# Kernel tuning notes

Measured on AMD Instinct MI355X. Metric: run time of the kernel, lower is better.

The kernel has to match this reference:

```python
import jax, jax.numpy as jnp
import numpy as np

Q = 12
DEGREE = 3
N_CONTROL = 25
N_POINTS = 500000
INPUT_DIM = 256


def make_open_uniform_knots(n_control, degree):
    n_knots = n_control + degree + 1
    n_internal = n_knots - 2 * (degree + 1)
    internal = np.linspace(0.0, 1.0, n_internal + 2)[1:-1]
    knots = np.concatenate([np.zeros(degree + 1), internal, np.ones(degree + 1)])
    return jnp.asarray(knots, dtype=jnp.float32)


def bspline_basis(x, knots, degree, n_basis):
    # x: [M] in [0,1]; returns [M, n_basis] via vectorized Cox-de Boor recursion
    x = jnp.clip(x, knots[0], knots[-1])
    xe = x[:, None]                      # [M,1]
    left = knots[:n_basis]
    right = knots[1:n_basis + 1]
    is_last = jnp.arange(n_basis) == (n_basis - 1)
    # degree-0 indicator; last interval is closed on the right
    N = jnp.where(is_last,
                  (xe >= left) & (xe <= right),
                  (xe >= left) & (xe < right)).astype(x.dtype)
    for p in range(1, degree + 1):
        d1 = knots[p:p + n_basis] - knots[:n_basis]
        d2 = knots[p + 1:p + 1 + n_basis] - knots[1:1 + n_basis]
        safe1 = jnp.where(d1 != 0, d1, 1.0)
        safe2 = jnp.where(d2 != 0, d2, 1.0)
        c1 = jnp.where(d1 != 0, (xe - knots[:n_basis]) / safe1, 0.0)
        c2 = jnp.where(d2 != 0, (knots[p + 1:p + 1 + n_basis] - xe) / safe2, 0.0)
        N_shift = jnp.concatenate([N[:, 1:], jnp.zeros_like(N[:, :1])], axis=1)
        N = c1 * N + c2 * N_shift
    return N


def setup_inputs() -> dict:
    key = jax.random.key(0)
    k0, k1, k2, k3 = jax.random.split(key, 4)
    emb = jax.random.normal(k0, (N_POINTS, INPUT_DIM), jnp.float32)
    W = jax.random.normal(k1, (Q, INPUT_DIM), jnp.float32) * 0.05
    b_inner = jnp.zeros((Q,), jnp.float32)
    inner_scale = jnp.full((1,), 0.5, jnp.float32)
    coeffs = jax.random.normal(k2, (Q, N_CONTROL), jnp.float32) * 0.05
    a = jax.random.normal(k3, (Q, 1), jnp.float32) * 0.05
    b_out = jnp.zeros((1,), jnp.float32)
    return {"emb": emb, "W": W, "b_inner": b_inner, "inner_scale": inner_scale,
            "coeffs": coeffs, "a": a, "b_out": b_out}


def reference(emb, W, b_inner, inner_scale, coeffs, a, b_out):
    knots = make_open_uniform_knots(N_CONTROL, DEGREE)  # constant buffer
    u_inner = emb @ W.T + b_inner                       # [N,Q]
    s = 0.5 * (jnp.tanh(inner_scale * u_inner) + 1.0)   # [N,Q] in (0,1)
    B_flat = bspline_basis(s.reshape(-1), knots, DEGREE, N_CONTROL)  # [N*Q, C]
    B = B_flat.reshape(emb.shape[0], Q, N_CONTROL)
    phi = jnp.einsum('nqc,qc->nq', B, coeffs)           # [N,Q]
    u_out = phi @ a + b_out                             # [N,1]
    return u_out
```

## Files before the change

kernel.cpp:

```cpp
#include <hip/hip_runtime.h>
#include <hip/hip_bf16.h>
#include <math.h>

#define NQ 12
#define DIMK 256
#define NCTRL 25
#define TPB 256
#define PTS_PER_BLK 256

__global__ __launch_bounds__(TPB, 4) void kan_bspline_kernel(
    const float* __restrict__ emb,
    const float* __restrict__ W,
    const float* __restrict__ b_inner,
    const float* __restrict__ inner_scale,
    const float* __restrict__ coeffs,
    const float* __restrict__ a_out,
    const float* __restrict__ b_out,
    float* __restrict__ out,
    int n)
{
    __shared__ __align__(16) float sW[NQ * DIMK];
    __shared__ float sC[NQ * NCTRL];

    for (int i = threadIdx.x; i < NQ * DIMK / 4; i += TPB)
        ((float4*)sW)[i] = ((const float4*)W)[i];
    for (int i = threadIdx.x; i < NQ * NCTRL; i += TPB)
        sC[i] = coeffs[i];
    __syncthreads();

    const int lane_r = threadIdx.x & 3;
    const int grp    = threadIdx.x >> 2;
    const int p0     = blockIdx.x * PTS_PER_BLK + grp * 4;
    const int nm1    = n - 1;

    float acc[NQ][4];
    #pragma unroll
    for (int q = 0; q < NQ; ++q)
        #pragma unroll
        for (int p = 0; p < 4; ++p)
            acc[q][p] = 0.0f;

    #pragma unroll 4
    for (int i = 0; i < 16; ++i) {
        const int k = lane_r * 4 + i * 16;
        float4 e[4];
        #pragma unroll
        for (int p = 0; p < 4; ++p) {
            int pi = p0 + p;
            pi = pi > nm1 ? nm1 : pi;
            e[p] = *(const float4*)(emb + (size_t)pi * DIMK + k);
        }
        #pragma unroll
        for (int q = 0; q < NQ; ++q) {
            float4 w = *(const float4*)(sW + q * DIMK + k);
            #pragma unroll
            for (int p = 0; p < 4; ++p) {
                acc[q][p] += e[p].x * w.x;
                acc[q][p] += e[p].y * w.y;
                acc[q][p] += e[p].z * w.z;
                acc[q][p] += e[p].w * w.w;
            }
        }
    }

    float u[NQ];
    #pragma unroll
    for (int q = 0; q < NQ; ++q) {
        float s0 = acc[q][0] + __shfl_xor(acc[q][0], 1);
        float s1 = acc[q][1] + __shfl_xor(acc[q][1], 1);
        float s2 = acc[q][2] + __shfl_xor(acc[q][2], 1);
        float s3 = acc[q][3] + __shfl_xor(acc[q][3], 1);
        float x = (lane_r & 1) ? s1 : s0;
        float y = (lane_r & 1) ? s3 : s2;
        x += __shfl_xor(x, 2);
        y += __shfl_xor(y, 2);
        u[q] = (lane_r & 2) ? y : x;
    }

    const int n_idx = p0 + lane_r;
    if (n_idx < n) {
        const float scale = inner_scale[0];
        const float h   = 1.0f / 22.0f;
        const float i1h = 22.0f;
        const float i2h = 11.0f;
        const float i3h = 22.0f / 3.0f;
        float result = b_out[0];

        for (int q = 0; q < NQ; ++q) {
            float uu = u[q] + b_inner[q];
            float s = 0.5f * tanhf(scale * uu) + 0.5f;

            int iv = (int)(s * 22.0f);
            iv = iv > 21 ? 21 : iv;
            iv = iv < 0 ? 0 : iv;
            float fiv = (float)iv;

            float l1 = s - fiv * h;
            float l2 = s - fmaxf(fiv - 1.0f, 0.0f) * h;
            float l3 = s - fmaxf(fiv - 2.0f, 0.0f) * h;
            float r1 = fminf((fiv + 1.0f) * h, 1.0f) - s;
            float r2 = fminf((fiv + 2.0f) * h, 1.0f) - s;
            float r3 = fminf((fiv + 3.0f) * h, 1.0f) - s;

            float inv_b = (iv >= 1) ? i2h : i1h;
            float inv_c = (iv <= 20) ? i2h : i1h;
            float inv_d = (iv >= 2) ? i3h : ((iv >= 1) ? i2h : i1h);
            float inv_e = (iv >= 1 && iv <= 20) ? i3h : i2h;
            float inv_f = (iv <= 19) ? i3h : ((iv <= 20) ? i2h : i1h);

            float temp, saved;
            temp = i1h;
            float N0 = r1 * temp;
            float N1 = l1 * temp;
            temp  = N0 * inv_b;
            N0    = r1 * temp;
            saved = l2 * temp;
            temp  = N1 * inv_c;
            N1    = saved + r2 * temp;
            float N2 = l1 * temp;
            temp  = N0 * inv_d;
            N0    = r1 * temp;
            saved = l3 * temp;
            temp  = N1 * inv_e;
            N1    = saved + r2 * temp;
            saved = l2 * temp;
            temp  = N2 * inv_f;
            N2    = saved + r3 * temp;
            float N3 = l1 * temp;

            const float* cq = sC + q * NCTRL + iv;
            float phi = N0 * cq[0] + N1 * cq[1] + N2 * cq[2] + N3 * cq[3];
            result += a_out[q] * phi;
        }
        out[n_idx] = result;
    }
}

extern "C" void kernel_launch(void* const* d_in, const int* in_sizes, int n_in,
                              void* d_out, int out_size, void* d_ws, size_t ws_size,
                              hipStream_t stream) {
    const float* emb         = (const float*)d_in[0];
    const float* W           = (const float*)d_in[1];
    const float* b_inner     = (const float*)d_in[2];
    const float* inner_scale = (const float*)d_in[3];
    const float* coeffs      = (const float*)d_in[4];
    const float* a_out       = (const float*)d_in[5];
    const float* b_out       = (const float*)d_in[6];
    float* out = (float*)d_out;

    const int n = in_sizes[0] / DIMK;
    const int blocks = (n + PTS_PER_BLK - 1) / PTS_PER_BLK;
    kan_bspline_kernel<<<blocks, TPB, 0, stream>>>(
        emb, W, b_inner, inner_scale, coeffs, a_out, b_out, out, n);
}
```

Before: 683.7 us.

## Persistent kernel with async global-to-LDS double buffering and DPP reductions

Turns the kernel into a persistent grid of at most 256 blocks. Each wave streams its own 16 rows of the embedding tile straight into double-buffered LDS with global_load_lds, so the next tile loads while the current one is computed. W is held in registers as float4s, and each 16-lane row computes a point's 12 dot products with DPP row reductions. The spline evaluation then runs in parallel across q lanes and finishes with a second DPP sum. Occupancy drops to one large-LDS block per CU, and the code relies on correct ordering from vmcnt waits.

```diff
diff --git a/kernel.cpp b/kernel.cpp
--- a/kernel.cpp
+++ b/kernel.cpp
@@ -1,14 +1,46 @@
 #include <hip/hip_runtime.h>
-#include <hip/hip_bf16.h>
 #include <math.h>
+#include <stdint.h>
 
 #define NQ 12
 #define DIMK 256
 #define NCTRL 25
 #define TPB 256
-#define PTS_PER_BLK 256
-
-__global__ __launch_bounds__(TPB, 4) void kan_bspline_kernel(
+#define TILE 64
+
+
+template<int CTRL>
+__device__ __forceinline__ float dpp_red(float v) {
+    int t = __builtin_amdgcn_mov_dpp(__float_as_int(v), CTRL, 0xF, 0xF, 1);
+    return v + __int_as_float(t);
+}
+
+__device__ __forceinline__ float row16_sum(float v) {
+    v = dpp_red<0xB1>(v);
+    v = dpp_red<0x4E>(v);
+    v = dpp_red<0x124>(v);
+    v = dpp_red<0x128>(v);
+    return v;
+}
+
+__device__ __forceinline__ void stage_tile(const float* __restrict__ emb,
+                                           float* dstbase, int p0,
+                                           int w, int lane, int nm1) {
+    #pragma unroll
+    for (int j = 0; j < 16; ++j) {
+        const int row = (w << 4) + j;
+        int grow = p0 + row;
+        grow = grow > nm1 ? nm1 : grow;
+        const float* src = emb + (size_t)grow * DIMK + (lane << 2);
+        float* dst = dstbase + row * DIMK;
+        __builtin_amdgcn_global_load_lds(
+            (const __attribute__((address_space(1))) void*)src,
+            (__attribute__((address_space(3))) void*)dst,
+            16, 0, 0);
+    }
+}
+
+__global__ __launch_bounds__(TPB, 1) void kan_bspline_kernel(
     const float* __restrict__ emb,
     const float* __restrict__ W,
     const float* __restrict__ b_inner,
@@ -19,120 +51,143 @@
     float* __restrict__ out,
     int n)
 {
-    __shared__ __align__(16) float sW[NQ * DIMK];
+    __shared__ __align__(16) float sE[2 * TILE * DIMK];
     __shared__ float sC[NQ * NCTRL];
 
-    for (int i = threadIdx.x; i < NQ * DIMK / 4; i += TPB)
-        ((float4*)sW)[i] = ((const float4*)W)[i];
-    for (int i = threadIdx.x; i < NQ * NCTRL; i += TPB)
-        sC[i] = coeffs[i];
+    const int tid  = threadIdx.x;
+    const int w    = tid >> 6;
+    const int lane = tid & 63;
+    const int cl   = lane >> 4;
+    const int h    = lane & 15;
+    const int nm1  = n - 1;
+    const int ntiles = (n + TILE - 1) / TILE;
+    const int G = (int)gridDim.x;
+
+    for (int i = tid; i < NQ * NCTRL; i += TPB) sC[i] = coeffs[i];
     __syncthreads();
 
-    const int lane_r = threadIdx.x & 3;
-    const int grp    = threadIdx.x >> 2;
-    const int p0     = blockIdx.x * PTS_PER_BLK + grp * 4;
-    const int nm1    = n - 1;
-
-    float acc[NQ][4];
+    float4 wq[NQ][4];
     #pragma unroll
     for (int q = 0; q < NQ; ++q)
         #pragma unroll
-        for (int p = 0; p < 4; ++p)
-            acc[q][p] = 0.0f;
-
-    #pragma unroll 4
-    for (int i = 0; i < 16; ++i) {
-        const int k = lane_r * 4 + i * 16;
-        float4 e[4];
+        for (int m = 0; m < 4; ++m)
+            wq[q][m] = *(const float4*)(W + q * DIMK + (m << 6) + (h << 2));
+
+    const float b_h = (h < NQ) ? b_inner[h] : 0.0f;
+    const float a_h = (h < NQ) ? a_out[h]   : 0.0f;
+    const float scale = inner_scale[0];
+    const float bout  = b_out[0];
+
+    const float hh  = 1.0f / 22.0f;
+    const float i1h = 22.0f;
+    const float i2h = 11.0f;
+    const float i3h = 22.0f / 3.0f;
+
+    int buf = 0;
+    const int t0 = blockIdx.x;
+    stage_tile(emb, sE, t0 * TILE, w, lane, nm1);
+    asm volatile("s_waitcnt vmcnt(0)" ::: "memory");
+
+    for (int t = t0; t < ntiles; t += G) {
+        const int tn = t + G;
+        if (tn < ntiles)
+            stage_tile(emb, sE + ((buf ^ 1) * (TILE * DIMK)), tn * TILE, w, lane, nm1);
+
+        const float* bp = sE + buf * (TILE * DIMK);
+        const int p0 = t * TILE;
+
         #pragma unroll
-        for (int p = 0; p < 4; ++p) {
-            int pi = p0 + p;
-            pi = pi > nm1 ? nm1 : pi;
-            e[p] = *(const float4*)(emb + (size_t)pi * DIMK + k);
-        }
-        #pragma unroll
-        for (int q = 0; q < NQ; ++q) {
-            float4 w = *(const float4*)(sW + q * DIMK + k);
+        for (int s = 0; s < 4; ++s) {
+            const int r = (w << 4) + (s << 2) + cl;
+            const float* ep = bp + r * DIMK + (h << 2);
+            const float4 e0 = *(const float4*)(ep);
+            const float4 e1 = *(const float4*)(ep + 64);
+            const float4 e2 = *(const float4*)(ep + 128);
+            const float4 e3 = *(const float4*)(ep + 192);
+
+            float red[NQ];
             #pragma unroll
-            for (int p = 0; p < 4; ++p) {
-                acc[q][p] += e[p].x * w.x;
-                acc[q][p] += e[p].y * w.y;
-                acc[q][p] += e[p].z * w.z;
-                acc[q][p] += e[p].w * w.w;
+            for (int q = 0; q < NQ; ++q) {
+                float acc;
+                acc  = e0.x * wq[q][0].x;
+                acc += e0.y * wq[q][0].y;
+                acc += e0.z * wq[q][0].z;
+                acc += e0.w * wq[q][0].w;
+                acc += e1.x * wq[q][1].x;
+                acc += e1.y * wq[q][1].y;
+                acc += e1.z * wq[q][1].z;
+                acc += e1.w * wq[q][1].w;
+                acc += e2.x * wq[q][2].x;
+                acc += e2.y * wq[q][2].y;
+                acc += e2.z * wq[q][2].z;
+                acc += e2.w * wq[q][2].w;
+                acc += e3.x * wq[q][3].x;
+                acc += e3.y * wq[q][3].y;
+                acc += e3.z * wq[q][3].z;
+                acc += e3.w * wq[q][3].w;
+                red[q] = row16_sum(acc);
+            }
+
+            float uq = 0.0f;
+            #pragma unroll
+            for (int q = 0; q < NQ; ++q) uq = (h == q) ? red[q] : uq;
+
+            const float uu = uq + b_h;
+            const float sv = 0.5f * tanhf(scale * uu) + 0.5f;
+
+            int iv = (int)(sv * 22.0f);
+            iv = iv > 21 ? 21 : iv;
+            iv = iv < 0 ? 0 : iv;
+            const float fiv = (float)iv;
+
+            const float l1 = sv - fiv * hh;
+            const float l2 = sv - fmaxf(fiv - 1.0f, 0.0f) * hh;
+            const float l3 = sv - fmaxf(fiv - 2.0f, 0.0f) * hh;
+            const float r1 = fminf((fiv + 1.0f) * hh, 1.0f) - sv;
+            const float r2 = fminf((fiv + 2.0f) * hh, 1.0f) - sv;
+            const float r3 = fminf((fiv + 3.0f) * hh, 1.0f) - sv;
+
+            const float inv_b = (iv >= 1) ? i2h : i1h;
+            const float inv_c = (iv <= 20) ? i2h : i1h;
+            const float inv_d = (iv >= 2) ? i3h : ((iv >= 1) ? i2h : i1h);
+            const float inv_e = (iv >= 1 && iv <= 20) ? i3h : i2h;
+            const float inv_f = (iv <= 19) ? i3h : ((iv <= 20) ? i2h : i1h);
+
+            float tmp, saved;
+            tmp = i1h;
+            float N0v = r1 * tmp;
+            float N1v = l1 * tmp;
+            tmp   = N0v * inv_b;
+            N0v   = r1 * tmp;
+            saved = l2 * tmp;
+            tmp   = N1v * inv_c;
+            N1v   = saved + r2 * tmp;
+            float N2v = l1 * tmp;
+            tmp   = N0v * inv_d;
+            N0v   = r1 * tmp;
+            saved = l3 * tmp;
+            tmp   = N1v * inv_e;
+            N1v   = saved + r2 * tmp;
+            saved = l2 * tmp;
+            tmp   = N2v * inv_f;
+            N2v   = saved + r3 * tmp;
+            float N3v = l1 * tmp;
+
+            const int qe = (h < NQ) ? h : 0;
+            const float* cq = sC + qe * NCTRL + iv;
+            const float phi = N0v * cq[0] + N1v * cq[1] + N2v * cq[2] + N3v * cq[3];
+
+            float part = a_h * phi;
+            part = row16_sum(part);
+
+            if (h == 0) {
+                const int pidx = p0 + r;
+                if (pidx < n) out[pidx] = part + bout;
             }
         }
-    }
-
-    float u[NQ];
-    #pragma unroll
-    for (int q = 0; q < NQ; ++q) {
-        float s0 = acc[q][0] + __shfl_xor(acc[q][0], 1);
-        float s1 = acc[q][1] + __shfl_xor(acc[q][1], 1);
-        float s2 = acc[q][2] + __shfl_xor(acc[q][2], 1);
-        float s3 = acc[q][3] + __shfl_xor(acc[q][3], 1);
-        float x = (lane_r & 1) ? s1 : s0;
-        float y = (lane_r & 1) ? s3 : s2;
-        x += __shfl_xor(x, 2);
-        y += __shfl_xor(y, 2);
-        u[q] = (lane_r & 2) ? y : x;
-    }
-
-    const int n_idx = p0 + lane_r;
-    if (n_idx < n) {
-        const float scale = inner_scale[0];
-        const float h   = 1.0f / 22.0f;
-        const float i1h = 22.0f;
-        const float i2h = 11.0f;
-        const float i3h = 22.0f / 3.0f;
-        float result = b_out[0];
-
-        for (int q = 0; q < NQ; ++q) {
-            float uu = u[q] + b_inner[q];
-            float s = 0.5f * tanhf(scale * uu) + 0.5f;
-
-            int iv = (int)(s * 22.0f);
-            iv = iv > 21 ? 21 : iv;
-            iv = iv < 0 ? 0 : iv;
-            float fiv = (float)iv;
-
-            float l1 = s - fiv * h;
-            float l2 = s - fmaxf(fiv - 1.0f, 0.0f) * h;
-            float l3 = s - fmaxf(fiv - 2.0f, 0.0f) * h;
-            float r1 = fminf((fiv + 1.0f) * h, 1.0f) - s;
-            float r2 = fminf((fiv + 2.0f) * h, 1.0f) - s;
-            float r3 = fminf((fiv + 3.0f) * h, 1.0f) - s;
-
-            float inv_b = (iv >= 1) ? i2h : i1h;
-            float inv_c = (iv <= 20) ? i2h : i1h;
-            float inv_d = (iv >= 2) ? i3h : ((iv >= 1) ? i2h : i1h);
-            float inv_e = (iv >= 1 && iv <= 20) ? i3h : i2h;
-            float inv_f = (iv <= 19) ? i3h : ((iv <= 20) ? i2h : i1h);
-
-            float temp, saved;
-            temp = i1h;
-            float N0 = r1 * temp;
-            float N1 = l1 * temp;
-            temp  = N0 * inv_b;
-            N0    = r1 * temp;
-            saved = l2 * temp;
-            temp  = N1 * inv_c;
-            N1    = saved + r2 * temp;
-            float N2 = l1 * temp;
-            temp  = N0 * inv_d;
-            N0    = r1 * temp;
-            saved = l3 * temp;
-            temp  = N1 * inv_e;
-            N1    = saved + r2 * temp;
-            saved = l2 * temp;
-            temp  = N2 * inv_f;
-            N2    = saved + r3 * temp;
-            float N3 = l1 * temp;
-
-            const float* cq = sC + q * NCTRL + iv;
-            float phi = N0 * cq[0] + N1 * cq[1] + N2 * cq[2] + N3 * cq[3];
-            result += a_out[q] * phi;
-        }
-        out[n_idx] = result;
+
+        asm volatile("s_waitcnt vmcnt(0)" ::: "memory");
+        buf ^= 1;
     }
 }
 
@@ -149,7 +204,8 @@
     float* out = (float*)d_out;
 
     const int n = in_sizes[0] / DIMK;
-    const int blocks = (n + PTS_PER_BLK - 1) / PTS_PER_BLK;
-    kan_bspline_kernel<<<blocks, TPB, 0, stream>>>(
+    const int ntiles = (n + TILE - 1) / TILE;
+    int grid = ntiles < 256 ? ntiles : 256;
+    kan_bspline_kernel<<<grid, TPB, 0, stream>>>(
         emb, W, b_inner, inner_scale, coeffs, a_out, b_out, out, n);
 }
```

Result: no change. 689.3 us (+0.8%).
